# Optimization experiments

Hardware: AMD Instinct MI355X
Metric: run time of the kernel (lower is better)

The kernel has to match this reference:

```python
import jax, jax.numpy as jnp
import numpy as np

B, C, H, W = 2, 64, 64, 64
C2 = C // 2
N = H * W


def conv1x1(x, w, b):
    # x: (B,Cin,H,W), w: (Cout,Cin), b: (Cout,)
    return jnp.einsum('bchw,oc->bohw', x, w) + b[None, :, None, None]


def setup_inputs() -> dict:
    key = jax.random.key(0)
    ks = jax.random.split(key, 20)
    s = 0.05
    d = {
        'x1': jax.random.normal(ks[0], (B, C, H, W), jnp.float32),
        'x2': jax.random.normal(ks[1], (B, C, H, W), jnp.float32),
        'wq1': jax.random.normal(ks[2], (C2, C), jnp.float32) * s,
        'bq1': jax.random.normal(ks[3], (C2,), jnp.float32) * s,
        'wk1': jax.random.normal(ks[4], (C2, C), jnp.float32) * s,
        'bk1': jax.random.normal(ks[5], (C2,), jnp.float32) * s,
        'wv1': jax.random.normal(ks[6], (C2, C), jnp.float32) * s,
        'bv1': jax.random.normal(ks[7], (C2,), jnp.float32) * s,
        'wc1': jax.random.normal(ks[8], (C, C2), jnp.float32) * s,
        'bc1': jax.random.normal(ks[9], (C,), jnp.float32) * s,
        'wq2': jax.random.normal(ks[10], (C2, C), jnp.float32) * s,
        'bq2': jax.random.normal(ks[11], (C2,), jnp.float32) * s,
        'wk2': jax.random.normal(ks[12], (C2, C), jnp.float32) * s,
        'bk2': jax.random.normal(ks[13], (C2,), jnp.float32) * s,
        'wv2': jax.random.normal(ks[14], (C2, C), jnp.float32) * s,
        'bv2': jax.random.normal(ks[15], (C2,), jnp.float32) * s,
        'wc2': jax.random.normal(ks[16], (C, C2), jnp.float32) * s,
        'bc2': jax.random.normal(ks[17], (C,), jnp.float32) * s,
        'gamma1': jax.random.normal(ks[18], (1,), jnp.float32) * 0.5,
        'gamma2': jax.random.normal(ks[19], (1,), jnp.float32) * 0.5,
    }
    return d


def reference(x1, x2, wq1, bq1, wk1, bk1, wv1, bv1, wc1, bc1,
              wq2, bq2, wk2, bk2, wv2, bv2, wc2, bc2, gamma1, gamma2):
    b, c, h, w = x1.shape
    n = h * w
    # branch-1 projections (boundary semantics)
    q1 = jnp.max(conv1x1(x1, wq1, bq1), axis=1).reshape(b, n)          # (B,N) channel-max
    k1 = jnp.max(conv1x1(x1, wk1, bk1).reshape(b, -1, n), axis=1)      # (B,N)
    v1 = conv1x1(x1, wv1, bv1).reshape(b, -1, n)                        # (B,C/2,N)
    # branch-2 projections (field semantics)
    q2 = jnp.mean(conv1x1(x2, wq2, bq2), axis=1).reshape(b, n)         # (B,N) channel-mean
    k2 = jnp.mean(conv1x1(x2, wk2, bk2).reshape(b, -1, n), axis=1)     # (B,N)
    v2 = conv1x1(x2, wv2, bv2).reshape(b, -1, n)                        # (B,C/2,N)
    # energy2 = q1 (B,N,1) @ k2 (B,1,N) outer product; inverted sigmoid gate
    att2 = 1.0 - jax.nn.sigmoid(q1[:, :, None] * k2[:, None, :])        # (B,N,N)
    out1 = jnp.einsum('bck,bmk->bcm', v1, att2).reshape(b, c // 2, h, w)
    out1 = conv1x1(out1, wc2, bc2)
    # energy1 = q2 outer k1; sigmoid gate
    att1 = jax.nn.sigmoid(q2[:, :, None] * k1[:, None, :])              # (B,N,N)
    out2 = jnp.einsum('bck,bmk->bcm', v2, att1).reshape(b, c // 2, h, w)
    out2 = conv1x1(out2, wc1, bc1)
    out1 = x1 + gamma1[0] * out1
    out2 = x2 + gamma2[0] * out2
    return (out1, out2)
```

## Files before the change

### kernel.cpp

```cpp
#include <hip/hip_runtime.h>
#include <hip/hip_bf16.h>

#define NN 4096
#define CC 64
#define C2 32
#define BB 2

#define M_BLK  16
#define KBLK   64
#define KB_ITERS (NN / KBLK)

#define WS_Q1 0
#define WS_K1 8192
#define WS_Q2 16384
#define WS_K2 24576
#define WS_V1 32768
#define WS_V2 163840

typedef __attribute__((address_space(1))) const unsigned int GUI;
typedef __attribute__((address_space(3))) unsigned int LUI;
typedef __attribute__((ext_vector_type(8))) short bf16x8;
typedef __attribute__((ext_vector_type(4))) float f32x4;

__device__ __forceinline__ void glds16(const void* g, void* l) {
    __builtin_amdgcn_global_load_lds((GUI*)g, (LUI*)l, 16, 0, 0);
}

__device__ __forceinline__ unsigned short bf16_rne(float f) {
    union { float f; unsigned u; } x; x.f = f;
    unsigned u = x.u + 0x7fff + ((x.u >> 16) & 1);
    return (unsigned short)(u >> 16);
}
__device__ __forceinline__ unsigned pack2(float a, float b) {
    __hip_bfloat162 h = __float22bfloat162_rn(make_float2(a, b));
    unsigned r; __builtin_memcpy(&r, &h, 4); return r;
}
__device__ __forceinline__ float sigm_e2(float x) {
    return __builtin_amdgcn_rcpf(1.0f + __builtin_amdgcn_exp2f(x));
}

__global__ __launch_bounds__(256) void proj_kernel(
    const float* __restrict__ x1, const float* __restrict__ x2,
    const float* __restrict__ wq1, const float* __restrict__ bq1,
    const float* __restrict__ wk1, const float* __restrict__ bk1,
    const float* __restrict__ wv1, const float* __restrict__ bv1,
    const float* __restrict__ wq2, const float* __restrict__ bq2,
    const float* __restrict__ wk2, const float* __restrict__ bk2,
    const float* __restrict__ wv2, const float* __restrict__ bv2,
    float* __restrict__ ws)
{
    const int ln = threadIdx.x & 63;
    const int og = threadIdx.x >> 6;
    const int n  = blockIdx.x * 64 + ln;
    const int p  = blockIdx.y;
    const int b  = blockIdx.z;

    const float* x; const float* w; const float* bias;
    int mode; float* dstf; unsigned short* dstv;
    switch (p) {
      case 0: x = x1; w = wq1; bias = bq1; mode = 0; dstf = ws + WS_Q1; dstv = 0; break;
      case 1: x = x1; w = wk1; bias = bk1; mode = 0; dstf = ws + WS_K1; dstv = 0; break;
      case 2: x = x1; w = wv1; bias = bv1; mode = 2; dstf = 0; dstv = (unsigned short*)(ws + WS_V1); break;
      case 3: x = x2; w = wq2; bias = bq2; mode = 1; dstf = ws + WS_Q2; dstv = 0; break;
      case 4: x = x2; w = wk2; bias = bk2; mode = 1; dstf = ws + WS_K2; dstv = 0; break;
      default:x = x2; w = wv2; bias = bv2; mode = 2; dstf = 0; dstv = (unsigned short*)(ws + WS_V2); break;
    }

    __shared__ float red[4][C2][64];

    float acc[C2];
    #pragma unroll
    for (int o = 0; o < C2; ++o) acc[o] = 0.0f;

    const float* xb = x + ((size_t)b * CC + og * 16) * NN + n;
    #pragma unroll
    for (int ci = 0; ci < 16; ++ci) {
        const float xv = xb[(size_t)ci * NN];
        #pragma unroll
        for (int o = 0; o < C2; ++o)
            acc[o] += w[o * CC + og * 16 + ci] * xv;
    }
    #pragma unroll
    for (int o = 0; o < C2; ++o) red[og][o][ln] = acc[o];
    __syncthreads();

    float f[8];
    #pragma unroll
    for (int j = 0; j < 8; ++j) {
        const int o = og * 8 + j;
        f[j] = red[0][o][ln] + red[1][o][ln] + red[2][o][ln] + red[3][o][ln]
             + bias[o];
    }

    if (mode == 2) {
        #pragma unroll
        for (int j = 0; j < 8; ++j)
            dstv[((size_t)b * C2 + og * 8 + j) * NN + n] = bf16_rne(f[j]);
    } else {
        float r;
        if (mode == 0) {
            r = f[0];
            #pragma unroll
            for (int j = 1; j < 8; ++j) r = fmaxf(r, f[j]);
        } else {
            r = 0.0f;
            #pragma unroll
            for (int j = 0; j < 8; ++j) r += f[j];
        }
        __syncthreads();
        red[og][0][ln] = r;
        __syncthreads();
        if (og == 0) {
            const float a0 = red[0][0][ln], a1 = red[1][0][ln];
            const float a2 = red[2][0][ln], a3 = red[3][0][ln];
            const float rr = (mode == 0)
                ? fmaxf(fmaxf(a0, a1), fmaxf(a2, a3))
                : (a0 + a1 + a2 + a3) * (1.0f / C2);
            dstf[(size_t)b * NN + n] = rr;
        }
    }
}

__global__ __launch_bounds__(256) void attn_mfma(
    const float* __restrict__ q1, const float* __restrict__ k1,
    const float* __restrict__ q2, const float* __restrict__ k2,
    const unsigned short* __restrict__ v1, const unsigned short* __restrict__ v2,
    const float* __restrict__ x1,  const float* __restrict__ x2,
    const float* __restrict__ wc1, const float* __restrict__ bc1,
    const float* __restrict__ wc2, const float* __restrict__ bc2,
    const float* __restrict__ g1,  const float* __restrict__ g2,
    float* __restrict__ out)
{
    __shared__ unsigned short vtile[2][C2 * KBLK];
    __shared__ unsigned short stile[2][M_BLK * KBLK];

    const int tid = threadIdx.x;
    const int wv  = tid >> 6;
    const int ln  = tid & 63;

    const int z      = blockIdx.y;
    const int branch = z & 1;
    const int b      = z >> 1;
    const int m0     = blockIdx.x * M_BLK;

    const float* q; const float* kv; const unsigned short* vbf; float sl2e;
    if (branch == 0) { q = q1; kv = k2; vbf = v1; sl2e =  1.44269504089f; }
    else             { q = q2; kv = k1; vbf = v2; sl2e = -1.44269504089f; }

    const int sm = tid & 15;
    const int sc = tid >> 4;
    const float qs = q[(size_t)b * NN + m0 + sm] * sl2e;
    const float* kvb = kv + (size_t)b * NN;

    f32x4 acc = (f32x4){0.f, 0.f, 0.f, 0.f};

    const int vc = tid >> 3;
    const int vs = tid & 7;
    const unsigned short* vsrc0 = vbf + (size_t)(b * C2 + vc) * NN
                                + ((vs ^ (vc & 7)) << 3);

    auto sigPackWrite = [&](int buf, float4 ka) {
        float s[4];
        s[0] = sigm_e2(qs * ka.x);  s[1] = sigm_e2(qs * ka.y);
        s[2] = sigm_e2(qs * ka.z);  s[3] = sigm_e2(qs * ka.w);

        uint2 w;
        w.x = pack2(s[0], s[1]); w.y = pack2(s[2], s[3]);

        char* srow = (char*)stile[buf] + sm * 128;
        *(uint2*)(srow + ((((sc >> 1) ^ (sm & 7)) << 4) + ((sc & 1) << 3))) = w;
    };

    glds16(vsrc0, (char*)vtile[0] + tid * 16);
    sigPackWrite(0, *(const float4*)(kvb + sc * 4));
    asm volatile("s_waitcnt vmcnt(0)" ::: "memory");
    __syncthreads();

    const int ct  = wv & 1;
    const int ks  = wv >> 1;
    const int col = (ks << 2) + (ln >> 4);
    const int ac  = ct * 16 + (ln & 15);
    const int bm  = ln & 15;

    for (int kb = 0; kb < KB_ITERS; ++kb) {
        const int cur = kb & 1;
        const bool more = (kb + 1 < KB_ITERS);

        float4 ka;
        if (more) {
            glds16(vsrc0 + (kb + 1) * KBLK,
                   (char*)vtile[cur ^ 1] + tid * 16);
            ka = *(const float4*)(kvb + (kb + 1) * KBLK + sc * 4);
        }

        const bf16x8 af = *(const bf16x8*)((const char*)vtile[cur]
                          + ac * 128 + ((col ^ (ac & 7)) << 4));
        const bf16x8 bfr = *(const bf16x8*)((const char*)stile[cur]
                           + bm * 128 + ((col ^ (bm & 7)) << 4));
        acc = __builtin_amdgcn_mfma_f32_16x16x32_bf16(af, bfr, acc, 0, 0, 0);

        if (more) sigPackWrite(cur ^ 1, ka);

        asm volatile("s_waitcnt vmcnt(0)" ::: "memory");
        __syncthreads();
    }

    float* red = (float*)stile;
    if (wv >= 2)
        *(f32x4*)&red[(wv - 2) * 256 + ln * 4] = acc;
    __syncthreads();
    float* s_lds = (float*)vtile;
    if (wv < 2) {
        const f32x4 o = *(const f32x4*)&red[wv * 256 + ln * 4];
        acc.x += o.x; acc.y += o.y; acc.z += o.z; acc.w += o.w;
        #pragma unroll
        for (int j = 0; j < 4; ++j) {
            const int c = wv * 16 + (ln >> 4) * 4 + j;
            s_lds[c * M_BLK + (ln & 15)] = acc[j];
        }
    }
    __syncthreads();

    const float* wmat; const float* bias; const float* x; float gamma;
    float* o;
    if (branch == 0) { wmat = wc2; bias = bc2; x = x1; gamma = g1[0]; o = out; }
    else             { wmat = wc1; bias = bc1; x = x2; gamma = g2[0];
                       o = out + (size_t)BB * CC * NN; }

    const int m  = tid & 15;
    const int ch = tid >> 4;

    float sv[C2];
    #pragma unroll
    for (int c = 0; c < C2; ++c) sv[c] = s_lds[c * M_BLK + m];

    #pragma unroll
    for (int j = 0; j < 4; ++j) {
        const int co = ch * 4 + j;
        float a = bias[co];
        #pragma unroll
        for (int c = 0; c < C2; ++c)
            a += wmat[co * C2 + c] * sv[c];
        const size_t idx = ((size_t)b * CC + co) * NN + m0 + m;
        o[idx] = x[idx] + gamma * a;
    }
}

extern "C" void kernel_launch(void* const* d_in, const int* in_sizes, int n_in,
                              void* d_out, int out_size, void* d_ws, size_t ws_size,
                              hipStream_t stream)
{
    const float* x1  = (const float*)d_in[0];
    const float* x2  = (const float*)d_in[1];
    const float* wq1 = (const float*)d_in[2];
    const float* bq1 = (const float*)d_in[3];
    const float* wk1 = (const float*)d_in[4];
    const float* bk1 = (const float*)d_in[5];
    const float* wv1 = (const float*)d_in[6];
    const float* bv1 = (const float*)d_in[7];
    const float* wc1 = (const float*)d_in[8];
    const float* bc1 = (const float*)d_in[9];
    const float* wq2 = (const float*)d_in[10];
    const float* bq2 = (const float*)d_in[11];
    const float* wk2 = (const float*)d_in[12];
    const float* bk2 = (const float*)d_in[13];
    const float* wv2 = (const float*)d_in[14];
    const float* bv2 = (const float*)d_in[15];
    const float* wc2 = (const float*)d_in[16];
    const float* bc2 = (const float*)d_in[17];
    const float* g1  = (const float*)d_in[18];
    const float* g2  = (const float*)d_in[19];

    float* ws  = (float*)d_ws;
    float* out = (float*)d_out;

    proj_kernel<<<dim3(NN / 64, 6, BB), 256, 0, stream>>>(
        x1, x2, wq1, bq1, wk1, bk1, wv1, bv1,
        wq2, bq2, wk2, bk2, wv2, bv2, ws);

    const float* q1 = ws + WS_Q1; const float* k1 = ws + WS_K1;
    const float* q2 = ws + WS_Q2; const float* k2 = ws + WS_K2;
    const unsigned short* v1 = (const unsigned short*)(ws + WS_V1);
    const unsigned short* v2 = (const unsigned short*)(ws + WS_V2);

    attn_mfma<<<dim3(NN / M_BLK, BB * 2), 256, 0, stream>>>(
        q1, k1, q2, k2, v1, v2,
        x1, x2, wc1, bc1, wc2, bc2, g1, g2, out);
}
```

Measured before the change: 57.90 us.

## Split key dimension across eight waves with direct global loads, drop LDS pipeline

After: 60.97 us. 5.3% more time.

```diff
diff --git a/kernel.cpp b/kernel.cpp
--- a/kernel.cpp
+++ b/kernel.cpp
@@ -5,10 +5,6 @@
 #define CC 64
 #define C2 32
 #define BB 2
-
-#define M_BLK  16
-#define KBLK   64
-#define KB_ITERS (NN / KBLK)
 
 #define WS_Q1 0
 #define WS_K1 8192
@@ -17,14 +13,8 @@
 #define WS_V1 32768
 #define WS_V2 163840
 
-typedef __attribute__((address_space(1))) const unsigned int GUI;
-typedef __attribute__((address_space(3))) unsigned int LUI;
 typedef __attribute__((ext_vector_type(8))) short bf16x8;
 typedef __attribute__((ext_vector_type(4))) float f32x4;
-
-__device__ __forceinline__ void glds16(const void* g, void* l) {
-    __builtin_amdgcn_global_load_lds((GUI*)g, (LUI*)l, 16, 0, 0);
-}
 
 __device__ __forceinline__ unsigned short bf16_rne(float f) {
     union { float f; unsigned u; } x; x.f = f;
@@ -121,7 +111,7 @@
     }
 }
 
-__global__ __launch_bounds__(256) void attn_mfma(
+__global__ __launch_bounds__(512) void attn_mfma(
     const float* __restrict__ q1, const float* __restrict__ k1,
     const float* __restrict__ q2, const float* __restrict__ k2,
     const unsigned short* __restrict__ v1, const unsigned short* __restrict__ v2,
@@ -131,8 +121,8 @@
     const float* __restrict__ g1,  const float* __restrict__ g2,
     float* __restrict__ out)
 {
-    __shared__ unsigned short vtile[2][C2 * KBLK];
-    __shared__ unsigned short stile[2][M_BLK * KBLK];
+    __shared__ float red[8][C2 * 16];
+    __shared__ float s_s[C2 * 16];
 
     const int tid = threadIdx.x;
     const int wv  = tid >> 6;
@@ -141,83 +131,59 @@
     const int z      = blockIdx.y;
     const int branch = z & 1;
     const int b      = z >> 1;
-    const int m0     = blockIdx.x * M_BLK;
+    const int m0     = blockIdx.x * 16;
 
     const float* q; const float* kv; const unsigned short* vbf; float sl2e;
     if (branch == 0) { q = q1; kv = k2; vbf = v1; sl2e =  1.44269504089f; }
     else             { q = q2; kv = k1; vbf = v2; sl2e = -1.44269504089f; }
 
-    const int sm = tid & 15;
-    const int sc = tid >> 4;
-    const float qs = q[(size_t)b * NN + m0 + sm] * sl2e;
+    const int m16 = ln & 15;
+    const int kg  = ln >> 4;
+    const float qs = q[(size_t)b * NN + m0 + m16] * sl2e;
     const float* kvb = kv + (size_t)b * NN;
 
-    f32x4 acc = (f32x4){0.f, 0.f, 0.f, 0.f};
-
-    const int vc = tid >> 3;
-    const int vs = tid & 7;
-    const unsigned short* vsrc0 = vbf + (size_t)(b * C2 + vc) * NN
-                                + ((vs ^ (vc & 7)) << 3);
-
-    auto sigPackWrite = [&](int buf, float4 ka) {
-        float s[4];
-        s[0] = sigm_e2(qs * ka.x);  s[1] = sigm_e2(qs * ka.y);
-        s[2] = sigm_e2(qs * ka.z);  s[3] = sigm_e2(qs * ka.w);
-
-        uint2 w;
-        w.x = pack2(s[0], s[1]); w.y = pack2(s[2], s[3]);
-
-        char* srow = (char*)stile[buf] + sm * 128;
-        *(uint2*)(srow + ((((sc >> 1) ^ (sm & 7)) << 4) + ((sc & 1) << 3))) = w;
-    };
-
-    glds16(vsrc0, (char*)vtile[0] + tid * 16);
-    sigPackWrite(0, *(const float4*)(kvb + sc * 4));
-    asm volatile("s_waitcnt vmcnt(0)" ::: "memory");
+    const int wk0 = wv * (NN / 8);
+    const unsigned short* vrow0 = vbf + (size_t)(b * C2 + m16) * NN;
+    const unsigned short* vrow1 = vbf + (size_t)(b * C2 + 16 + m16) * NN;
+
+    f32x4 acc0 = (f32x4){0.f, 0.f, 0.f, 0.f};
+    f32x4 acc1 = (f32x4){0.f, 0.f, 0.f, 0.f};
+
+    #pragma unroll 2
+    for (int it = 0; it < (NN / 8) / 32; ++it) {
+        const int k0 = wk0 + it * 32 + kg * 8;
+
+        const bf16x8 a0 = *(const bf16x8*)(vrow0 + k0);
+        const bf16x8 a1 = *(const bf16x8*)(vrow1 + k0);
+        const float4 kfa = *(const float4*)(kvb + k0);
+        const float4 kfb = *(const float4*)(kvb + k0 + 4);
+
+        const float s0 = sigm_e2(qs * kfa.x), s1 = sigm_e2(qs * kfa.y);
+        const float s2 = sigm_e2(qs * kfa.z), s3 = sigm_e2(qs * kfa.w);
+        const float s4 = sigm_e2(qs * kfb.x), s5 = sigm_e2(qs * kfb.y);
+        const float s6 = sigm_e2(qs * kfb.z), s7 = sigm_e2(qs * kfb.w);
+
+        uint4 wB;
+        wB.x = pack2(s0, s1); wB.y = pack2(s2, s3);
+        wB.z = pack2(s4, s5); wB.w = pack2(s6, s7);
+        bf16x8 bf; __builtin_memcpy(&bf, &wB, 16);
+
+        acc0 = __builtin_amdgcn_mfma_f32_16x16x32_bf16(a0, bf, acc0, 0, 0, 0);
+        acc1 = __builtin_amdgcn_mfma_f32_16x16x32_bf16(a1, bf, acc1, 0, 0, 0);
+    }
+
+    #pragma unroll
+    for (int j = 0; j < 4; ++j) {
+        red[wv][(kg * 4 + j) * 16 + m16]      = acc0[j];
+        red[wv][(16 + kg * 4 + j) * 16 + m16] = acc1[j];
+    }
     __syncthreads();
 
-    const int ct  = wv & 1;
-    const int ks  = wv >> 1;
-    const int col = (ks << 2) + (ln >> 4);
-    const int ac  = ct * 16 + (ln & 15);
-    const int bm  = ln & 15;
-
-    for (int kb = 0; kb < KB_ITERS; ++kb) {
-        const int cur = kb & 1;
-        const bool more = (kb + 1 < KB_ITERS);
-
-        float4 ka;
-        if (more) {
-            glds16(vsrc0 + (kb + 1) * KBLK,
-                   (char*)vtile[cur ^ 1] + tid * 16);
-            ka = *(const float4*)(kvb + (kb + 1) * KBLK + sc * 4);
-        }
-
-        const bf16x8 af = *(const bf16x8*)((const char*)vtile[cur]
-                          + ac * 128 + ((col ^ (ac & 7)) << 4));
-        const bf16x8 bfr = *(const bf16x8*)((const char*)stile[cur]
-                           + bm * 128 + ((col ^ (bm & 7)) << 4));
-        acc = __builtin_amdgcn_mfma_f32_16x16x32_bf16(af, bfr, acc, 0, 0, 0);
-
-        if (more) sigPackWrite(cur ^ 1, ka);
-
-        asm volatile("s_waitcnt vmcnt(0)" ::: "memory");
-        __syncthreads();
-    }
-
-    float* red = (float*)stile;
-    if (wv >= 2)
-        *(f32x4*)&red[(wv - 2) * 256 + ln * 4] = acc;
-    __syncthreads();
-    float* s_lds = (float*)vtile;
-    if (wv < 2) {
-        const f32x4 o = *(const f32x4*)&red[wv * 256 + ln * 4];
-        acc.x += o.x; acc.y += o.y; acc.z += o.z; acc.w += o.w;
-        #pragma unroll
-        for (int j = 0; j < 4; ++j) {
-            const int c = wv * 16 + (ln >> 4) * 4 + j;
-            s_lds[c * M_BLK + (ln & 15)] = acc[j];
-        }
+    {
+        float s = 0.0f;
+        #pragma unroll
+        for (int w8 = 0; w8 < 8; ++w8) s += red[w8][tid];
+        s_s[tid] = s;
     }
     __syncthreads();
 
@@ -227,16 +193,16 @@
     else             { wmat = wc1; bias = bc1; x = x2; gamma = g2[0];
                        o = out + (size_t)BB * CC * NN; }
 
-    const int m  = tid & 15;
-    const int ch = tid >> 4;
+    const int m   = tid & 15;
+    const int co0 = tid >> 4;
 
     float sv[C2];
     #pragma unroll
-    for (int c = 0; c < C2; ++c) sv[c] = s_lds[c * M_BLK + m];
-
-    #pragma unroll
-    for (int j = 0; j < 4; ++j) {
-        const int co = ch * 4 + j;
+    for (int c = 0; c < C2; ++c) sv[c] = s_s[c * 16 + m];
+
+    #pragma unroll
+    for (int rep = 0; rep < 2; ++rep) {
+        const int co = co0 + rep * 32;
         float a = bias[co];
         #pragma unroll
         for (int c = 0; c < C2; ++c)
@@ -283,7 +249,7 @@
     const unsigned short* v1 = (const unsigned short*)(ws + WS_V1);
     const unsigned short* v2 = (const unsigned short*)(ws + WS_V2);
 
-    attn_mfma<<<dim3(NN / M_BLK, BB * 2), 256, 0, stream>>>(
+    attn_mfma<<<dim3(NN / 16, BB * 2), 512, 0, stream>>>(
         q1, k1, q2, k2, v1, v2,
         x1, x2, wc1, bc1, wc2, bc2, g1, g2, out);
 }
```
